# Optimization experiments

Measured on AMD Instinct MI355X. Metric: run time of the kernel, lower is better.

Reference implementation:

```python
import jax, jax.numpy as jnp
import numpy as np

NUM_BINS = 3
TAIL_BOUND = 1.0


def conv3x3(x, w, b):
    # x: [B,C,H,W], w: [O,I,3,3]
    y = jax.lax.conv_general_dilated(x, w, (1, 1), 'SAME',
                                     dimension_numbers=('NCHW', 'OIHW', 'NCHW'))
    return y + b[None, :, None, None]


def unconstrained_linear_spline(inputs, unnormalized_pdf, tail_bound=TAIL_BOUND):
    # inputs: [B,C,H,W]; unnormalized_pdf: [B,C,H,W,num_bins]
    num_bins = unnormalized_pdf.shape[-1]
    left = bottom = -tail_bound
    right = top = tail_bound
    inside = (inputs >= left) & (inputs <= right)

    x = (inputs - left) / (right - left)  # scale to [0,1]
    pdf = jax.nn.softmax(unnormalized_pdf, axis=-1)
    cdf = jnp.cumsum(pdf, axis=-1)
    cdf = cdf.at[..., -1].set(1.0)
    cdf = jnp.pad(cdf, [(0, 0)] * (cdf.ndim - 1) + [(1, 0)])  # [..., num_bins+1]

    pos = jnp.clip(x, 0.0, 1.0) * num_bins  # clip keeps bin idx valid for outside elems
    bin_idx = jnp.clip(jnp.floor(pos).astype(jnp.int32), 0, num_bins - 1)
    alpha = pos - bin_idx.astype(pos.dtype)

    input_pdfs = jnp.take_along_axis(pdf, bin_idx[..., None], axis=-1)[..., 0]
    out = jnp.take_along_axis(cdf, bin_idx[..., None], axis=-1)[..., 0] + alpha * input_pdfs
    out = jnp.clip(out, 0.0, 1.0)
    lad = jnp.log(input_pdfs) + jnp.log(jnp.asarray(num_bins, pos.dtype))

    out = out * (top - bottom) + bottom
    lad = lad - jnp.log(jnp.asarray(top - bottom, pos.dtype)) + jnp.log(jnp.asarray(right - left, pos.dtype))

    out = jnp.where(inside, out, inputs)       # identity tails
    lad = jnp.where(inside, lad, 0.0)
    return out, lad


def setup_inputs() -> dict:
    key = jax.random.key(0)
    ks = jax.random.split(key, 4)
    B, C, H, W = 32, 64, 64, 64
    hidden = 128
    c_half = C // 2
    c_out = c_half * NUM_BINS
    x = jax.random.normal(ks[0], (B, C, H, W), dtype=jnp.float32)
    objective = jnp.zeros((B,), dtype=jnp.float32)
    W1 = jax.random.normal(ks[1], (hidden, c_half, 3, 3), dtype=jnp.float32) * 0.05
    b1 = jnp.zeros((hidden,), dtype=jnp.float32)
    W2 = jax.random.normal(ks[2], (c_out, hidden, 3, 3), dtype=jnp.float32) * 0.05
    b2 = jnp.zeros((c_out,), dtype=jnp.float32)
    return {'x': x, 'objective': objective, 'W1': W1, 'b1': b1, 'W2': W2, 'b2': b2}


def reference(x, objective, W1, b1, W2, b2):
    identity_split, transform_split = jnp.split(x, 2, axis=1)
    h = jax.nn.relu(conv3x3(identity_split, W1, b1))
    transform_params = conv3x3(h, W2, b2)  # [B, C/2*num_bins, H, W]
    b, c, hh, ww = transform_split.shape
    transform_params = transform_params.reshape(b, c, NUM_BINS, hh, ww).transpose(0, 1, 3, 4, 2)
    transformed, logabsdet = unconstrained_linear_spline(transform_split, transform_params)
    output = jnp.concatenate([identity_split, transformed], axis=1)
    objective_out = objective + jnp.sum(logabsdet.reshape(b, -1), axis=1)
    return output, objective_out
```

## Files before the change

### kernel.cpp

```cpp
#include <hip/hip_runtime.h>

typedef __attribute__((ext_vector_type(8))) __bf16 bf16x8;
typedef __attribute__((ext_vector_type(4))) float f32x4;

__device__ __forceinline__ unsigned short f2bf(float f) {
    unsigned int u = __builtin_bit_cast(unsigned int, f);
    u = (u + 0x7FFFu + ((u >> 16) & 1u)) >> 16;
    return (unsigned short)u;
}

__global__ void __launch_bounds__(256) prep_w(const float* __restrict__ W1,
                                              const float* __restrict__ W2,
                                              unsigned short* __restrict__ Wt1,
                                              unsigned short* __restrict__ Wt2) {
    int tid = blockIdx.x * 256 + threadIdx.x;
    if (tid < 36864) {
        int tt = tid % 9, rem = tid / 9;
        int i = rem & 31, o = rem >> 5;
        Wt1[(tt * 128 + o) * 32 + i] = f2bf(W1[tid]);
    }
    if (tid < 110592) {
        int tt = tid % 9, rem = tid / 9;
        int i = rem & 127, o = rem >> 7;
        int kc = i >> 6, ii = i & 63;
        int khalf = ii >> 5, kgrp = (ii >> 3) & 3, j = ii & 7;
        int o_tile = o >> 4, lrow = o & 15;
        int s = kc * 9 + tt;
        Wt2[(size_t)s * 6144 +
            (size_t)(((o_tile * 2 + khalf) * 64 + kgrp * 16 + lrow) * 8 + j)] = f2bf(W2[tid]);
    }
}

__global__ void __launch_bounds__(256) conv1_fused(const float* __restrict__ x,
                                                   const float* __restrict__ obj,
                                                   const float* __restrict__ b1,
                                                   const unsigned short* __restrict__ Wt1,
                                                   unsigned short* __restrict__ hbuf,
                                                   float* __restrict__ out) {
    const int LW = 40;
    __shared__ unsigned short sx[6 * 66 * LW];
    int wg = blockIdx.x;
    int b = wg >> 4, h0 = (wg & 15) << 2;
    int t = threadIdx.x;

#pragma unroll
    for (int j = 0; j < 8; ++j) {
        int idx = j * 256 + t;
        int c = idx >> 6, row = (idx >> 4) & 3, w4 = idx & 15;
        size_t off = (((size_t)b * 64 + c) * 64 + (h0 + row)) * 16 + w4;
        reinterpret_cast<float4*>(out)[off] =
            reinterpret_cast<const float4*>(x)[off];
    }
    if (wg == 0 && t < 32) out[8388608 + t] = obj[t];

    if (t < 48) {
        int row = t >> 3, k = t & 7;
        int col = (k & 1) ? 65 : 0, c0 = (k >> 1) * 8;
        *reinterpret_cast<uint4*>(&sx[(row * 66 + col) * LW + c0]) = uint4{0, 0, 0, 0};
    }
    {
        int w = t & 63, c2 = (t >> 6) * 2;
        const float* xb = x + (size_t)b * 262144;
#pragma unroll
        for (int row = 0; row < 6; ++row) {
            int gh = h0 - 1 + row;
            unsigned short* srow = &sx[(row * 66 + w + 1) * LW];
            if (gh >= 0 && gh < 64) {
                const float* xr = xb + (size_t)gh * 64;
#pragma unroll
                for (int co = 0; co < 4; ++co) {
                    int c = co * 8 + c2;
                    float f0 = xr[(size_t)c * 4096 + w];
                    float f1 = xr[(size_t)(c + 1) * 4096 + w];
                    unsigned pk = (unsigned)f2bf(f0) | ((unsigned)f2bf(f1) << 16);
                    *reinterpret_cast<unsigned*>(&srow[c]) = pk;
                }
            } else {
#pragma unroll
                for (int co = 0; co < 4; ++co) {
                    int c = co * 8 + c2;
                    *reinterpret_cast<unsigned*>(&srow[c]) = 0u;
                }
            }
        }
    }
    __syncthreads();

    int wid = t >> 6, lane = t & 63;
    int lrow = lane & 15, kgrp = lane >> 4;

    bf16x8 afr[2][9];
#pragma unroll
    for (int m2 = 0; m2 < 2; ++m2) {
        int o = (wid * 2 + m2) * 16 + lrow;
#pragma unroll
        for (int tap = 0; tap < 9; ++tap)
            afr[m2][tap] = *reinterpret_cast<const bf16x8*>(
                Wt1 + (size_t)(tap * 128 + o) * 32 + kgrp * 8);
    }

    for (int nt = 0; nt < 16; ++nt) {
        int r = nt >> 2, ww = ((nt & 3) << 4) + lrow;
        f32x4 acc0 = {0.f, 0.f, 0.f, 0.f}, acc1 = {0.f, 0.f, 0.f, 0.f};
#pragma unroll
        for (int dh = 0; dh < 3; ++dh)
#pragma unroll
            for (int dw = 0; dw < 3; ++dw) {
                int tap = dh * 3 + dw;
                bf16x8 bfr = *reinterpret_cast<const bf16x8*>(
                    &sx[((r + dh) * 66 + ww + dw) * LW + kgrp * 8]);
                acc0 = __builtin_amdgcn_mfma_f32_16x16x32_bf16(afr[0][tap], bfr, acc0, 0, 0, 0);
                acc1 = __builtin_amdgcn_mfma_f32_16x16x32_bf16(afr[1][tap], bfr, acc1, 0, 0, 0);
            }
        int hh = h0 + r;
        size_t obase = (((size_t)b * 64 + hh) * 64 + ww) * 128;
#pragma unroll
        for (int m2 = 0; m2 < 2; ++m2) {
            f32x4 a = (m2 == 0) ? acc0 : acc1;
            int o0 = (wid * 2 + m2) * 16 + kgrp * 4;
            unsigned short r4[4];
#pragma unroll
            for (int j = 0; j < 4; ++j) {
                float v = a[j] + b1[o0 + j];
                r4[j] = f2bf(fmaxf(v, 0.f));
            }
            uint2 pk;
            pk.x = (unsigned)r4[0] | ((unsigned)r4[1] << 16);
            pk.y = (unsigned)r4[2] | ((unsigned)r4[3] << 16);
            *reinterpret_cast<uint2*>(hbuf + obase + o0) = pk;
        }
    }
}

__global__ void __launch_bounds__(512) conv2_spline(const unsigned short* __restrict__ hbuf,
                                                    const float* __restrict__ b2,
                                                    const unsigned short* __restrict__ Wt2,
                                                    const float* __restrict__ x,
                                                    float* __restrict__ out) {
    const int LWA = 72;
    __shared__ __align__(16) unsigned short sa[6 * 66 * LWA];
    __shared__ float red[8];
    float* pm = reinterpret_cast<float*>(sa);

    int raw = blockIdx.x;
    int wg = (raw & 7) * 64 + (raw >> 3);
    int b = wg >> 4, h0 = (wg & 15) << 2;
    int t = threadIdx.x;
    int wid = t >> 6, lane = t & 63;
    int lrow = lane & 15, kgrp = lane >> 4;
    int mgrp = wid >> 2, ngrp = wid & 3;
    int mb = mgrp * 3;

    f32x4 acc[3][4];
#pragma unroll
    for (int i = 0; i < 3; ++i)
#pragma unroll
        for (int j = 0; j < 4; ++j) acc[i][j] = f32x4{0.f, 0.f, 0.f, 0.f};

    const unsigned short* wfb = Wt2 + (size_t)lane * 8;

    for (int kc2 = 0; kc2 < 2; ++kc2) {
        if (kc2) __syncthreads();
#pragma unroll
        for (int j = 0; j < 6; ++j) {
            int idx = j * 512 + t;
            int row = idx >> 9, rem = idx & 511;
            int w = rem >> 3, c0 = (rem & 7) * 8;
            int gh = h0 - 1 + row;
            uint4 v = uint4{0, 0, 0, 0};
            if (gh >= 0 && gh < 64)
                v = *reinterpret_cast<const uint4*>(
                    hbuf + (((size_t)b * 64 + gh) * 64 + w) * 128 + kc2 * 64 + c0);
            *reinterpret_cast<uint4*>(&sa[(row * 66 + (w + 1)) * LWA + c0]) = v;
        }
        if (t < 96) {
            int row = t >> 4, k = t & 15;
            int col = (k & 1) ? 65 : 0, c0 = (k >> 1) * 8;
            *reinterpret_cast<uint4*>(&sa[(row * 66 + col) * LWA + c0]) = uint4{0, 0, 0, 0};
        }
        __syncthreads();

#pragma unroll
        for (int tap = 0; tap < 9; ++tap) {
            int s = kc2 * 9 + tap;
            const unsigned short* wsl = wfb + (size_t)s * 6144;
            int dh = tap / 3, dw = tap % 3;
            bf16x8 wfr[3][2];
#pragma unroll
            for (int mi = 0; mi < 3; ++mi) {
                int ot = mb + mi;
                wfr[mi][0] = *reinterpret_cast<const bf16x8*>(wsl + (size_t)(ot * 2 + 0) * 512);
                wfr[mi][1] = *reinterpret_cast<const bf16x8*>(wsl + (size_t)(ot * 2 + 1) * 512);
            }
#pragma unroll
            for (int ni = 0; ni < 4; ++ni) {
                int nt = ngrp * 4 + ni;
                int rr = nt >> 2, wcol = (nt & 3) * 16 + lrow;
                int base = ((rr + dh) * 66 + wcol + dw) * LWA;
                bf16x8 a0 = *reinterpret_cast<const bf16x8*>(&sa[base + kgrp * 8]);
                bf16x8 a1 = *reinterpret_cast<const bf16x8*>(&sa[base + 32 + kgrp * 8]);
#pragma unroll
                for (int mi = 0; mi < 3; ++mi) {
                    acc[mi][ni] = __builtin_amdgcn_mfma_f32_16x16x32_bf16(wfr[mi][0], a0, acc[mi][ni], 0, 0, 0);
                    acc[mi][ni] = __builtin_amdgcn_mfma_f32_16x16x32_bf16(wfr[mi][1], a1, acc[mi][ni], 0, 0, 0);
                }
            }
        }
    }

    float lad_acc = 0.f;
    for (int half = 0; half < 2; ++half) {
        __syncthreads();
        if ((ngrp >> 1) == half) {
#pragma unroll
            for (int mi = 0; mi < 3; ++mi) {
                int o0 = (mb + mi) * 16 + kgrp * 4;
                float bb0 = b2[o0], bb1 = b2[o0 + 1], bb2 = b2[o0 + 2], bb3 = b2[o0 + 3];
#pragma unroll
                for (int ni = 0; ni < 4; ++ni) {
                    int p = (ngrp & 1) * 64 + ni * 16 + lrow;
                    f32x4 v = acc[mi][ni];
                    pm[p * 101 + o0]     = v[0] + bb0;
                    pm[p * 101 + o0 + 1] = v[1] + bb1;
                    pm[p * 101 + o0 + 2] = v[2] + bb2;
                    pm[p * 101 + o0 + 3] = v[3] + bb3;
                }
            }
        }
        __syncthreads();
#pragma unroll 4
        for (int it = 0; it < 8; ++it) {
            int idx = it * 512 + t;
            int c = idx >> 7, p = idx & 127;
            int pos = half * 128 + p;
            int pb = p * 101 + 3 * c;
            float u0 = pm[pb];
            float u1 = pm[pb + 1];
            float u2 = pm[pb + 2];
            size_t gpos = (size_t)(b * 64 + 32 + c) * 4096 + (size_t)(h0 + (pos >> 6)) * 64 + (pos & 63);
            float xin = x[gpos];
            float mx = fmaxf(u0, fmaxf(u1, u2));
            float e0 = __expf(u0 - mx), e1 = __expf(u1 - mx), e2 = __expf(u2 - mx);
            float s = e0 + e1 + e2;
            float inv = 1.0f / s;
            float pos01 = fminf(fmaxf((xin + 1.f) * 0.5f, 0.f), 1.f) * 3.f;
            int bin = (int)pos01; bin = bin > 2 ? 2 : bin;
            float alpha = pos01 - (float)bin;
            float eb = (bin == 0) ? e0 : ((bin == 1) ? e1 : e2);
            float cb = (bin == 0) ? 0.f : ((bin == 1) ? e0 : (e0 + e1));
            float pk = eb * inv;
            float outv = cb * inv + alpha * pk;
            outv = fminf(fmaxf(outv, 0.f), 1.f) * 2.f - 1.f;
            float lad = __logf(pk) + 1.09861228866810969f;
            bool inside = (xin >= -1.f) && (xin <= 1.f);
            if (!inside) { outv = xin; lad = 0.f; }
            out[gpos] = outv;
            lad_acc += lad;
        }
    }
#pragma unroll
    for (int off = 32; off > 0; off >>= 1)
        lad_acc += __shfl_down(lad_acc, off, 64);
    if (lane == 0) red[wid] = lad_acc;
    __syncthreads();
    if (t == 0) {
        float s = 0.f;
#pragma unroll
        for (int i = 0; i < 8; ++i) s += red[i];
        atomicAdd(out + 8388608 + b, s);
    }
}

extern "C" void kernel_launch(void* const* d_in, const int* in_sizes, int n_in,
                              void* d_out, int out_size, void* d_ws, size_t ws_size,
                              hipStream_t stream) {
    const float* x   = (const float*)d_in[0];
    const float* obj = (const float*)d_in[1];
    const float* W1  = (const float*)d_in[2];
    const float* b1  = (const float*)d_in[3];
    const float* W2  = (const float*)d_in[4];
    const float* b2  = (const float*)d_in[5];
    float* out = (float*)d_out;
    char* ws = (char*)d_ws;

    unsigned short* hbuf = (unsigned short*)ws;
    unsigned short* Wt1  = (unsigned short*)(ws + 33554432);
    unsigned short* Wt2  = (unsigned short*)(ws + 33554432 + 73728);

    hipLaunchKernelGGL(prep_w,       dim3(432), dim3(256), 0, stream, W1, W2, Wt1, Wt2);
    hipLaunchKernelGGL(conv1_fused,  dim3(512), dim3(256), 0, stream, x, obj, b1, Wt1, hbuf, out);
    hipLaunchKernelGGL(conv2_spline, dim3(512), dim3(512), 0, stream, hbuf, b2, Wt2, x, out);
}
```

Measured before the change: 73.72 us.

## Fuse weight preparation into conv1 kernel, dropping separate prep launch

Removes the separate prep_w launch. The W2 bf16 repacking now runs in 432 extra blocks appended to the conv1 grid, and each conv1 workgroup builds its W1 MFMA fragments directly from fp32 W1 with on-the-fly bf16 conversion. This cuts one kernel launch and the dependency gap before conv1. The cost is strided scalar fp32 loads of W1 in every conv1 block, and the extra blocks compete with conv1 work for CUs.

```diff
diff --git a/kernel.cpp b/kernel.cpp
--- a/kernel.cpp
+++ b/kernel.cpp
@@ -9,39 +9,38 @@
     return (unsigned short)u;
 }
 
-__global__ void __launch_bounds__(256) prep_w(const float* __restrict__ W1,
-                                              const float* __restrict__ W2,
-                                              unsigned short* __restrict__ Wt1,
-                                              unsigned short* __restrict__ Wt2) {
-    int tid = blockIdx.x * 256 + threadIdx.x;
-    if (tid < 36864) {
-        int tt = tid % 9, rem = tid / 9;
-        int i = rem & 31, o = rem >> 5;
-        Wt1[(tt * 128 + o) * 32 + i] = f2bf(W1[tid]);
-    }
-    if (tid < 110592) {
-        int tt = tid % 9, rem = tid / 9;
-        int i = rem & 127, o = rem >> 7;
-        int kc = i >> 6, ii = i & 63;
-        int khalf = ii >> 5, kgrp = (ii >> 3) & 3, j = ii & 7;
-        int o_tile = o >> 4, lrow = o & 15;
-        int s = kc * 9 + tt;
-        Wt2[(size_t)s * 6144 +
-            (size_t)(((o_tile * 2 + khalf) * 64 + kgrp * 16 + lrow) * 8 + j)] = f2bf(W2[tid]);
-    }
-}
-
 __global__ void __launch_bounds__(256) conv1_fused(const float* __restrict__ x,
                                                    const float* __restrict__ obj,
+                                                   const float* __restrict__ W1,
+                                                   const float* __restrict__ W2,
                                                    const float* __restrict__ b1,
-                                                   const unsigned short* __restrict__ Wt1,
+                                                   unsigned short* __restrict__ Wt2,
                                                    unsigned short* __restrict__ hbuf,
                                                    float* __restrict__ out) {
     const int LW = 40;
     __shared__ unsigned short sx[6 * 66 * LW];
-    int wg = blockIdx.x;
-    int b = wg >> 4, h0 = (wg & 15) << 2;
+    int wb = blockIdx.x;
     int t = threadIdx.x;
+
+    if (wb >= 512) {
+        int tid = (wb - 512) * 256 + t;
+        if (tid < 32) out[8388608 + tid] = obj[tid];
+        if (tid < 110592) {
+            int tt = tid % 9, rem = tid / 9;
+            int i = rem & 127, o = rem >> 7;
+            int kc = i >> 6, ii = i & 63;
+            int khalf = ii >> 5, kgrp2 = (ii >> 3) & 3, j = ii & 7;
+            int o_tile = o >> 4, lrow2 = o & 15;
+            int s = kc * 9 + tt;
+            Wt2[(size_t)s * 6144 +
+                (size_t)(((o_tile * 2 + khalf) * 64 + kgrp2 * 16 + lrow2) * 8 + j)] = f2bf(W2[tid]);
+        }
+        return;
+    }
+
+    int b = wb >> 4, h0 = (wb & 15) << 2;
+    int wid = t >> 6, lane = t & 63;
+    int lrow = lane & 15, kgrp = lane >> 4;
 
 #pragma unroll
     for (int j = 0; j < 8; ++j) {
@@ -51,7 +50,22 @@
         reinterpret_cast<float4*>(out)[off] =
             reinterpret_cast<const float4*>(x)[off];
     }
-    if (wg == 0 && t < 32) out[8388608 + t] = obj[t];
+
+    bf16x8 afr[2][9];
+#pragma unroll
+    for (int m2 = 0; m2 < 2; ++m2) {
+        int o = (wid * 2 + m2) * 16 + lrow;
+        const float* w1o = W1 + (size_t)o * 288 + (size_t)kgrp * 72;
+#pragma unroll
+        for (int tap = 0; tap < 9; ++tap) {
+            uint4 pk;
+            pk.x = (unsigned)f2bf(w1o[0 * 9 + tap]) | ((unsigned)f2bf(w1o[1 * 9 + tap]) << 16);
+            pk.y = (unsigned)f2bf(w1o[2 * 9 + tap]) | ((unsigned)f2bf(w1o[3 * 9 + tap]) << 16);
+            pk.z = (unsigned)f2bf(w1o[4 * 9 + tap]) | ((unsigned)f2bf(w1o[5 * 9 + tap]) << 16);
+            pk.w = (unsigned)f2bf(w1o[6 * 9 + tap]) | ((unsigned)f2bf(w1o[7 * 9 + tap]) << 16);
+            afr[m2][tap] = __builtin_bit_cast(bf16x8, pk);
+        }
+    }
 
     if (t < 48) {
         int row = t >> 3, k = t & 7;
@@ -85,19 +99,6 @@
         }
     }
     __syncthreads();
-
-    int wid = t >> 6, lane = t & 63;
-    int lrow = lane & 15, kgrp = lane >> 4;
-
-    bf16x8 afr[2][9];
-#pragma unroll
-    for (int m2 = 0; m2 < 2; ++m2) {
-        int o = (wid * 2 + m2) * 16 + lrow;
-#pragma unroll
-        for (int tap = 0; tap < 9; ++tap)
-            afr[m2][tap] = *reinterpret_cast<const bf16x8*>(
-                Wt1 + (size_t)(tap * 128 + o) * 32 + kgrp * 8);
-    }
 
     for (int nt = 0; nt < 16; ++nt) {
         int r = nt >> 2, ww = ((nt & 3) << 4) + lrow;
@@ -284,10 +285,10 @@
     char* ws = (char*)d_ws;
 
     unsigned short* hbuf = (unsigned short*)ws;
-    unsigned short* Wt1  = (unsigned short*)(ws + 33554432);
-    unsigned short* Wt2  = (unsigned short*)(ws + 33554432 + 73728);
-
-    hipLaunchKernelGGL(prep_w,       dim3(432), dim3(256), 0, stream, W1, W2, Wt1, Wt2);
-    hipLaunchKernelGGL(conv1_fused,  dim3(512), dim3(256), 0, stream, x, obj, b1, Wt1, hbuf, out);
-    hipLaunchKernelGGL(conv2_spline, dim3(512), dim3(512), 0, stream, hbuf, b2, Wt2, x, out);
-}
+    unsigned short* Wt2  = (unsigned short*)(ws + 33554432);
+
+    hipLaunchKernelGGL(conv1_fused,  dim3(944), dim3(256), 0, stream,
+                       x, obj, W1, W2, b1, Wt2, hbuf, out);
+    hipLaunchKernelGGL(conv2_spline, dim3(512), dim3(512), 0, stream,
+                       hbuf, b2, Wt2, x, out);
+}
```

Measured after the change: 74.18 us. Within noise of the previous version (+0.6%).
